# Performance work log

Hardware: AMD Instinct MI355X
Metric: run time of the kernel (lower is better)

The kernel has to match this reference:

```python
import jax, jax.numpy as jnp
import numpy as np

EPS = 1e-6
N_HEADS = 16
N_KV_HEADS = 4
HEAD_DIM = 128
DIM = 2048
SEQ = 2048
BATCH = 2


def _make_freqs_cis(seqlen, head_dim, theta=10000.0):
    inv = 1.0 / (theta ** (jnp.arange(0, head_dim, 2, dtype=jnp.float32) / head_dim))  # [hd/2]
    t = jnp.arange(seqlen, dtype=jnp.float32)
    ang = jnp.outer(t, inv)  # [seq, hd/2]
    return jnp.stack([jnp.cos(ang), jnp.sin(ang)], axis=-1)  # [seq, hd/2, 2]


def setup_inputs() -> dict:
    key = jax.random.key(0)
    k1, k2, k3 = jax.random.split(key, 3)
    std = 0.02
    x = jax.random.normal(k1, (BATCH, SEQ, DIM), dtype=jnp.float32)
    freqs_cis = _make_freqs_cis(SEQ, HEAD_DIM)
    norm_w = jnp.ones((DIM,), dtype=jnp.float32)
    wqkv_w = jax.random.normal(k2, ((N_HEADS + 2 * N_KV_HEADS) * HEAD_DIM, DIM), dtype=jnp.float32) * std
    wo_w = jax.random.normal(k3, (DIM, N_HEADS * HEAD_DIM), dtype=jnp.float32) * std
    return {"x": x, "freqs_cis": freqs_cis, "norm_w": norm_w, "wqkv_w": wqkv_w, "wo_w": wo_w}


def _rope(t, cos, sin):
    # t: [b, s, h, hd] viewed as pairs; cos/sin: [s, hd/2]
    b, s, h, hd = t.shape
    tr = t.reshape(b, s, h, hd // 2, 2)
    xr, xi = tr[..., 0], tr[..., 1]
    c = cos[None, :, None, :]
    sn = sin[None, :, None, :]
    out_r = xr * c - xi * sn
    out_i = xr * sn + xi * c
    return jnp.stack([out_r, out_i], axis=-1).reshape(b, s, h, hd)


def reference(x, freqs_cis, norm_w, wqkv_w, wo_w):
    bs, seqlen, dim = x.shape
    n_rep = N_HEADS // N_KV_HEADS
    # RMSNorm
    xn = x * jax.lax.rsqrt(jnp.mean(x * x, axis=-1, keepdims=True) + EPS) * norm_w
    # fused QKV projection
    qkv = jnp.einsum('bsd,ed->bse', xn, wqkv_w)
    q_sz = N_HEADS * HEAD_DIM
    kv_sz = N_KV_HEADS * HEAD_DIM
    xq = qkv[..., :q_sz].reshape(bs, seqlen, N_HEADS, HEAD_DIM)
    xk = qkv[..., q_sz:q_sz + kv_sz].reshape(bs, seqlen, N_KV_HEADS, HEAD_DIM)
    xv = qkv[..., q_sz + kv_sz:].reshape(bs, seqlen, N_KV_HEADS, HEAD_DIM)
    cos, sin = freqs_cis[..., 0], freqs_cis[..., 1]
    xq = _rope(xq, cos, sin)
    xk = _rope(xk, cos, sin)
    # GQA: group q heads so kv broadcast replaces repeat_kv materialization
    q = xq.transpose(0, 2, 1, 3).reshape(bs, N_KV_HEADS, n_rep, seqlen, HEAD_DIM)
    k = xk.transpose(0, 2, 1, 3)  # [b, g, s, d]
    v = xv.transpose(0, 2, 1, 3)
    scale = 1.0 / jnp.sqrt(jnp.float32(HEAD_DIM))
    scores = jnp.einsum('bgrqd,bgkd->bgrqk', q, k) * scale
    causal = jnp.tril(jnp.ones((seqlen, seqlen), dtype=bool))
    scores = jnp.where(causal, scores, jnp.finfo(scores.dtype).min)
    probs = jax.nn.softmax(scores, axis=-1)
    out = jnp.einsum('bgrqk,bgkd->bgrqd', probs, v)
    out = out.reshape(bs, N_HEADS, seqlen, HEAD_DIM).transpose(0, 2, 1, 3).reshape(bs, seqlen, N_HEADS * HEAD_DIM)
    return jnp.einsum('bse,de->bsd', out, wo_w)
```

## Files before the change

### kernel.cpp

```cpp
#include <hip/hip_runtime.h>
#include <cstdint>
#include <cstddef>

typedef __bf16 bhalf;
typedef __bf16 bhalf8 __attribute__((ext_vector_type(8)));
typedef __bf16 bhalf4 __attribute__((ext_vector_type(4)));
typedef float f32x4 __attribute__((ext_vector_type(4)));
typedef float f32x16 __attribute__((ext_vector_type(16)));

#define RMS_EPS 1e-6f
#define N_HEADS 16
#define N_KV 4
#define HD 128
#define DIM 2048
#define SEQ 2048
#define BATCH 2

static __device__ __forceinline__ f32x4 mfma16(bhalf8 a, bhalf8 b, f32x4 c) {
    return __builtin_amdgcn_mfma_f32_16x16x32_bf16(a, b, c, 0, 0, 0);
}
static __device__ __forceinline__ f32x16 mfma32(bhalf8 a, bhalf8 b, f32x16 c) {
    return __builtin_amdgcn_mfma_f32_32x32x16_bf16(a, b, c, 0, 0, 0);
}

static __device__ __forceinline__ void gload16(const bhalf* g, bhalf* l) {
    __builtin_amdgcn_global_load_lds((const __attribute__((address_space(1))) unsigned int*)g,
                                     (__attribute__((address_space(3))) unsigned int*)l,
                                     16, 0, 0);
}

static __device__ __forceinline__ unsigned cvt_pk_bf16(float a, float b) {
    unsigned r;
    asm volatile("v_cvt_pk_bf16_f32 %0, %1, %2" : "=v"(r) : "v"(a), "v"(b));
    return r;
}
static __device__ __forceinline__ void plane32_swap(unsigned& a, unsigned& b) {
    asm volatile("v_permlane32_swap_b32 %0, %1" : "+v"(a), "+v"(b));
}

__global__ __launch_bounds__(256) void cvt_w(const float* __restrict__ a,
                                             const float* __restrict__ b,
                                             bhalf* __restrict__ dst) {
    size_t i = ((size_t)blockIdx.x * 256 + threadIdx.x) * 4;
    const size_t NQ = (size_t)3072 * 2048;
    float4 v = (i < NQ) ? ((const float4*)a)[i >> 2] : ((const float4*)b)[(i - NQ) >> 2];
    bhalf4 o;
    o[0] = (bhalf)v.x; o[1] = (bhalf)v.y; o[2] = (bhalf)v.z; o[3] = (bhalf)v.w;
    *(bhalf4*)(dst + i) = o;
}

__global__ __launch_bounds__(256) void rmsnorm_k(const float* __restrict__ x,
                                                 const float* __restrict__ w,
                                                 bhalf* __restrict__ xn) {
    const int row = blockIdx.x;
    const int tid = threadIdx.x;
    const float4* xr = (const float4*)(x + (size_t)row * DIM);
    float4 v0 = xr[tid * 2], v1 = xr[tid * 2 + 1];
    float ss = v0.x * v0.x + v0.y * v0.y + v0.z * v0.z + v0.w * v0.w
             + v1.x * v1.x + v1.y * v1.y + v1.z * v1.z + v1.w * v1.w;
    #pragma unroll
    for (int off = 32; off; off >>= 1) ss += __shfl_xor(ss, off, 64);
    __shared__ float red[4];
    if ((tid & 63) == 0) red[tid >> 6] = ss;
    __syncthreads();
    float tot = red[0] + red[1] + red[2] + red[3];
    float scale = rsqrtf(tot * (1.0f / DIM) + RMS_EPS);
    const float4* wr = (const float4*)w;
    float4 w0 = wr[tid * 2], w1 = wr[tid * 2 + 1];
    bhalf8 o;
    o[0] = (bhalf)(v0.x * scale * w0.x); o[1] = (bhalf)(v0.y * scale * w0.y);
    o[2] = (bhalf)(v0.z * scale * w0.z); o[3] = (bhalf)(v0.w * scale * w0.w);
    o[4] = (bhalf)(v1.x * scale * w1.x); o[5] = (bhalf)(v1.y * scale * w1.y);
    o[6] = (bhalf)(v1.z * scale * w1.z); o[7] = (bhalf)(v1.w * scale * w1.w);
    *(bhalf8*)(xn + (size_t)row * DIM + tid * 8) = o;
}

template <typename OutT>
__global__ __launch_bounds__(256) void gemm_abt(const bhalf* __restrict__ A,
                                                const bhalf* __restrict__ B,
                                                OutT* __restrict__ C,
                                                int N, int K) {
    const int tid = threadIdx.x;
    const int wave = tid >> 6, lane = tid & 63;
    const int quad = lane >> 4, r16 = lane & 15;
    const int m0 = blockIdx.y * 128, n0 = blockIdx.x * 128;
    const int wm = (wave >> 1) * 64, wn = (wave & 1) * 64;

    __shared__ __align__(16) bhalf sA[128][32];
    __shared__ __align__(16) bhalf sB[128][32];

    f32x4 acc[4][4];
    #pragma unroll
    for (int i = 0; i < 4; ++i)
        #pragma unroll
        for (int j = 0; j < 4; ++j) acc[i][j] = (f32x4)0.0f;

    const int lrow = lane >> 2;
    const int lcol = (lane & 3) * 8;
    const int arow = 32 * wave + lrow;
    const bhalf* Ap = A + (size_t)(m0 + arow) * K + lcol;
    const bhalf* Bp = B + (size_t)(n0 + arow) * K + lcol;
    const size_t rs16 = (size_t)16 * K;
    bhalf* sAp0 = &sA[32 * wave][0];
    bhalf* sAp1 = &sA[32 * wave + 16][0];
    bhalf* sBp0 = &sB[32 * wave][0];
    bhalf* sBp1 = &sB[32 * wave + 16][0];

    for (int k0 = 0; k0 < K; k0 += 32) {
        __syncthreads();
        gload16(Ap + k0, sAp0);
        gload16(Ap + k0 + rs16, sAp1);
        gload16(Bp + k0, sBp0);
        gload16(Bp + k0 + rs16, sBp1);
        __syncthreads();
        bhalf8 af[4], bfr[4];
        #pragma unroll
        for (int i = 0; i < 4; ++i) af[i]  = *(bhalf8*)&sA[wm + i * 16 + r16][quad * 8];
        #pragma unroll
        for (int j = 0; j < 4; ++j) bfr[j] = *(bhalf8*)&sB[wn + j * 16 + r16][quad * 8];
        #pragma unroll
        for (int i = 0; i < 4; ++i)
            #pragma unroll
            for (int j = 0; j < 4; ++j)
                acc[i][j] = mfma16(af[i], bfr[j], acc[i][j]);
    }

    #pragma unroll
    for (int i = 0; i < 4; ++i) {
        const int rbase = m0 + wm + i * 16 + quad * 4;
        #pragma unroll
        for (int rr = 0; rr < 4; ++rr) {
            OutT* crow = C + (size_t)(rbase + rr) * N + n0 + wn + r16;
            #pragma unroll
            for (int j = 0; j < 4; ++j) crow[j * 16] = (OutT)acc[i][j][rr];
        }
    }
}

__global__ __launch_bounds__(256) void rope_k(const bhalf* __restrict__ qkv,
                                              const float* __restrict__ freqs,
                                              bhalf* __restrict__ qb,
                                              bhalf* __restrict__ kb,
                                              bhalf* __restrict__ vt) {
    const int bs = blockIdx.x;
    const int b = bs >> 11, s = bs & 2047;
    const bhalf* row = qkv + (size_t)bs * 3072;
    const int tid = threadIdx.x;

    {
        const int h = tid >> 4, d20 = (tid & 15) * 4;
        bhalf8 e = *(const bhalf8*)(row + h * HD + d20 * 2);
        const float* fp = freqs + (size_t)s * 128 + d20 * 2;
        float4 f0 = *(const float4*)fp;
        float4 f1 = *(const float4*)(fp + 4);
        bhalf8 o;
        o[0] = (bhalf)((float)e[0] * f0.x - (float)e[1] * f0.y);
        o[1] = (bhalf)((float)e[0] * f0.y + (float)e[1] * f0.x);
        o[2] = (bhalf)((float)e[2] * f0.z - (float)e[3] * f0.w);
        o[3] = (bhalf)((float)e[2] * f0.w + (float)e[3] * f0.z);
        o[4] = (bhalf)((float)e[4] * f1.x - (float)e[5] * f1.y);
        o[5] = (bhalf)((float)e[4] * f1.y + (float)e[5] * f1.x);
        o[6] = (bhalf)((float)e[6] * f1.z - (float)e[7] * f1.w);
        o[7] = (bhalf)((float)e[6] * f1.w + (float)e[7] * f1.z);
        *(bhalf8*)(qb + ((size_t)(b * N_HEADS + h) * SEQ + s) * HD + d20 * 2) = o;
    }
    if (tid < 64) {
        const int kh = tid >> 4, d20 = (tid & 15) * 4;
        bhalf8 e = *(const bhalf8*)(row + 2048 + kh * HD + d20 * 2);
        const float* fp = freqs + (size_t)s * 128 + d20 * 2;
        float4 f0 = *(const float4*)fp;
        float4 f1 = *(const float4*)(fp + 4);
        bhalf8 o;
        o[0] = (bhalf)((float)e[0] * f0.x - (float)e[1] * f0.y);
        o[1] = (bhalf)((float)e[0] * f0.y + (float)e[1] * f0.x);
        o[2] = (bhalf)((float)e[2] * f0.z - (float)e[3] * f0.w);
        o[3] = (bhalf)((float)e[2] * f0.w + (float)e[3] * f0.z);
        o[4] = (bhalf)((float)e[4] * f1.x - (float)e[5] * f1.y);
        o[5] = (bhalf)((float)e[4] * f1.y + (float)e[5] * f1.x);
        o[6] = (bhalf)((float)e[6] * f1.z - (float)e[7] * f1.w);
        o[7] = (bhalf)((float)e[6] * f1.w + (float)e[7] * f1.z);
        *(bhalf8*)(kb + ((size_t)(b * N_KV + kh) * SEQ + s) * HD + d20 * 2) = o;
    }
    for (int e = tid; e < 512; e += 256) {
        const int kh = e >> 7, d = e & 127;
        vt[((size_t)(b * N_KV + kh) * HD + d) * SEQ + s] = row[2560 + e];
    }
}

__global__ __launch_bounds__(256, 2) void attn_k(const bhalf* __restrict__ qb,
                                                 const bhalf* __restrict__ kb,
                                                 const bhalf* __restrict__ vt,
                                                 bhalf* __restrict__ ob) {
    const int tid = threadIdx.x;
    const int wave = tid >> 6, lane = tid & 63;
    const int l31 = lane & 31, h2 = lane >> 5;
    const int qw = wave & 1, kw = wave >> 1;
    const int bid = ((blockIdx.x & 7) << 6) | ((int)blockIdx.x >> 3);
    const int pair = bid & 15;
    const int hh = (bid >> 4) & 15;
    const int b = bid >> 8;
    const int kvh = hh >> 2;

    __shared__ __align__(16) char smem[33792];
    char* const sK = smem;
    char* const sV = smem + 16384;
    float* const mrg = (float*)smem;

    const bhalf* Kbase = kb + (size_t)(b * N_KV + kvh) * SEQ * HD;
    const bhalf* Vbase = vt + (size_t)(b * N_KV + kvh) * HD * SEQ;
    const float SCL2 = 0.08838834764831845f * 1.4426950408889634f;

    const int mbase = (qw * 64 + lane) * 66;
    const int kr = tid >> 4, kce = (tid & 15) * 8;
    const int vr = tid >> 3, vce = (tid & 7) * 8;
    const int kcB = kce * 2, vcB = vce * 2;
    const int Xl = (h2 << 4) ^ ((l31 & 7) << 4);

    for (int phase = 0; phase < 2; ++phase) {
        const int qt = phase ? (31 - pair) : pair;
        const int qrow = qt * 64 + qw * 32 + l31;
        const int qhi = qt * 64 + qw * 32 + 31;

        const bhalf* qbase = qb + (((size_t)(b * N_HEADS + hh) * SEQ) + qrow) * HD;
        bhalf8 qf[8];
        #pragma unroll
        for (int kk = 0; kk < 8; ++kk) {
            bhalf8 q0 = *(const bhalf8*)(qbase + kk * 16 + h2 * 8);
            #pragma unroll
            for (int e = 0; e < 8; ++e) q0[e] = (bhalf)((float)q0[e] * SCL2);
            qf[kk] = q0;
        }

        f32x16 accO[4];
        #pragma unroll
        for (int dt = 0; dt < 4; ++dt) accO[dt] = (f32x16)0.0f;
        float m_i = -1e30f, l_i = 0.0f;

        bhalf8 kreg[4], vreg[4];
        #pragma unroll
        for (int i = 0; i < 4; ++i) {
            kreg[i] = *(const bhalf8*)(Kbase + (size_t)(kr + 16 * i) * HD + kce);
            vreg[i] = *(const bhalf8*)(Vbase + (size_t)(vr + 32 * i) * SEQ + vce);
        }

        for (int kt = 0; kt <= qt; ++kt) {
            __syncthreads();
            #pragma unroll
            for (int i = 0; i < 4; ++i) {
                const int rk = kr + 16 * i;
                *(bhalf8*)(sK + rk * 256 + (kcB ^ ((rk & 7) << 4))) = kreg[i];
                const int rv = vr + 32 * i;
                *(bhalf8*)(sV + rv * 128 + (vcB ^ ((rv & 7) << 4))) = vreg[i];
            }
            __syncthreads();
            if (kt < qt) {
                const int kn = (kt + 1) * 64;
                #pragma unroll
                for (int i = 0; i < 4; ++i) {
                    kreg[i] = *(const bhalf8*)(Kbase + (size_t)(kn + kr + 16 * i) * HD + kce);
                    vreg[i] = *(const bhalf8*)(Vbase + (size_t)(vr + 32 * i) * SEQ + kn + vce);
                }
            }
            if (qhi < kt * 64 + kw * 32) continue;

            f32x16 accS = (f32x16)0.0f;
            const char* kRow = sK + (kw * 32 + l31) * 256;
            #pragma unroll
            for (int kk = 0; kk < 8; ++kk)
                accS = mfma32(*(const bhalf8*)(kRow + ((kk * 32) ^ Xl)), qf[kk], accS);

            if (kt == qt) {
                #pragma unroll
                for (int r = 0; r < 16; ++r) {
                    const int key = kt * 64 + kw * 32 + (r & 3) + 8 * (r >> 2) + 4 * h2;
                    if (key > qrow) accS[r] = -1e30f;
                }
            }

            float mx = -1e30f;
            #pragma unroll
            for (int r = 0; r < 16; ++r) mx = fmaxf(mx, accS[r]);
            mx = fmaxf(mx, __shfl_xor(mx, 32, 64));

            if (!__all(mx <= m_i + 8.0f)) {
                const float mnew = fmaxf(m_i, mx);
                const float alpha = __builtin_amdgcn_exp2f(m_i - mnew);
                m_i = mnew;
                l_i *= alpha;
                #pragma unroll
                for (int dt = 0; dt < 4; ++dt)
                    #pragma unroll
                    for (int r = 0; r < 16; ++r) accO[dt][r] *= alpha;
            }

            float p[16];
            float rs = 0.0f;
            #pragma unroll
            for (int r = 0; r < 16; ++r) {
                p[r] = __builtin_amdgcn_exp2f(accS[r] - m_i);
                rs += p[r];
            }
            rs += __shfl_xor(rs, 32, 64);
            l_i += rs;

            unsigned X0 = cvt_pk_bf16(p[0],  p[1]);
            unsigned X1 = cvt_pk_bf16(p[2],  p[3]);
            unsigned X2 = cvt_pk_bf16(p[4],  p[5]);
            unsigned X3 = cvt_pk_bf16(p[6],  p[7]);
            unsigned X4 = cvt_pk_bf16(p[8],  p[9]);
            unsigned X5 = cvt_pk_bf16(p[10], p[11]);
            unsigned X6 = cvt_pk_bf16(p[12], p[13]);
            unsigned X7 = cvt_pk_bf16(p[14], p[15]);
            plane32_swap(X0, X2);
            plane32_swap(X1, X3);
            plane32_swap(X4, X6);
            plane32_swap(X5, X7);
            union { unsigned u[8]; bhalf8 h[2]; } pk;
            pk.u[0] = X0; pk.u[1] = X1; pk.u[2] = X2; pk.u[3] = X3;
            pk.u[4] = X4; pk.u[5] = X5; pk.u[6] = X6; pk.u[7] = X7;

            #pragma unroll
            for (int kk2 = 0; kk2 < 2; ++kk2) {
                const int cb = (kw << 6) | (kk2 << 5);
                #pragma unroll
                for (int dt = 0; dt < 4; ++dt) {
                    const bhalf8 vfv = *(const bhalf8*)(sV + (dt * 32 + l31) * 128 + (cb ^ Xl));
                    accO[dt] = mfma32(vfv, pk.h[kk2], accO[dt]);
                }
            }
        }

        __syncthreads();
        if (kw == 1) {
            #pragma unroll
            for (int dt = 0; dt < 4; ++dt)
                #pragma unroll
                for (int r = 0; r < 16; ++r) mrg[mbase + dt * 16 + r] = accO[dt][r];
            mrg[mbase + 64] = m_i;
            mrg[mbase + 65] = l_i;
        }
        __syncthreads();
        if (kw == 0) {
            const float m1 = mrg[mbase + 64];
            const float l1 = mrg[mbase + 65];
            const float m = fmaxf(m_i, m1);
            const float b0 = __builtin_amdgcn_exp2f(m_i - m);
            const float b1 = __builtin_amdgcn_exp2f(m1 - m);
            const float inv = 1.0f / (l_i * b0 + l1 * b1);
            bhalf* obase = ob + ((size_t)b * SEQ + qrow) * (size_t)(N_HEADS * HD) + hh * HD;
            #pragma unroll
            for (int dt = 0; dt < 4; ++dt)
                #pragma unroll
                for (int c = 0; c < 4; ++c) {
                    bhalf4 o4;
                    #pragma unroll
                    for (int rr = 0; rr < 4; ++rr) {
                        const float v = accO[dt][c * 4 + rr] * b0 +
                                        mrg[mbase + dt * 16 + c * 4 + rr] * b1;
                        o4[rr] = (bhalf)(v * inv);
                    }
                    *(bhalf4*)(obase + dt * 32 + c * 8 + h2 * 4) = o4;
                }
        }
    }
}

extern "C" void kernel_launch(void* const* d_in, const int* in_sizes, int n_in,
                              void* d_out, int out_size, void* d_ws, size_t ws_size,
                              hipStream_t stream) {
    const float* x      = (const float*)d_in[0];
    const float* freqs  = (const float*)d_in[1];
    const float* norm_w = (const float*)d_in[2];
    const float* wqkv   = (const float*)d_in[3];
    const float* wo     = (const float*)d_in[4];
    float* out = (float*)d_out;

    char* ws = (char*)d_ws;
    bhalf* wqkv_b = (bhalf*)(ws);
    bhalf* wo_b   = (bhalf*)(ws + 12582912);
    bhalf* xn     = (bhalf*)(ws + 20971520);
    bhalf* qkv    = (bhalf*)(ws + 37748736);
    bhalf* qb     = (bhalf*)(ws + 88080384);
    bhalf* kb     = (bhalf*)(ws + 104857600);
    bhalf* vtb    = (bhalf*)(ws + 109051904);
    bhalf* attn   = (bhalf*)(ws + 113246208);

    cvt_w<<<10240, 256, 0, stream>>>(wqkv, wo, wqkv_b);
    rmsnorm_k<<<BATCH * SEQ, 256, 0, stream>>>(x, norm_w, xn);
    gemm_abt<bhalf><<<dim3(24, 32), 256, 0, stream>>>(xn, wqkv_b, qkv, 3072, 2048);
    rope_k<<<BATCH * SEQ, 256, 0, stream>>>(qkv, freqs, qb, kb, vtb);
    attn_k<<<512, 256, 0, stream>>>(qb, kb, vtb, attn);
    gemm_abt<float><<<dim3(16, 32), 256, 0, stream>>>(attn, wo_b, out, 2048, 2048);
}
```

Before: 319.5 us.

## Replace GEMM with 256x256-tile, 512-thread, triple-buffered pipelined kernel

Replaces the 128x128 single-buffered GEMM with a 256x256-tile kernel using 8 waves, a three-stage LDS ring with asynchronous global-to-LDS loads, XOR-swizzled LDS addressing, and block-index remapping for L2 locality. Loads for future k-steps overlap the MFMA work, and s_setprio raises priority during the MFMA bursts. The aim is to raise arithmetic intensity and hide memory latency in the QKV and output projections. Larger tiles mean only 192 and 128 blocks, which may underfill the GPU's compute units, and the kernel needs 96KB of dynamic shared memory.

```diff
diff --git a/kernel.cpp b/kernel.cpp
--- a/kernel.cpp
+++ b/kernel.cpp
@@ -76,61 +76,99 @@
 }
 
 template <typename OutT>
-__global__ __launch_bounds__(256) void gemm_abt(const bhalf* __restrict__ A,
-                                                const bhalf* __restrict__ B,
-                                                OutT* __restrict__ C,
-                                                int N, int K) {
+__global__ __launch_bounds__(512) void gemm256(const bhalf* __restrict__ A,
+                                               const bhalf* __restrict__ B,
+                                               OutT* __restrict__ C,
+                                               int N, int K) {
+    extern __shared__ __align__(16) char smem[];
     const int tid = threadIdx.x;
-    const int wave = tid >> 6, lane = tid & 63;
+    const int wid = tid >> 6, lane = tid & 63;
     const int quad = lane >> 4, r16 = lane & 15;
-    const int m0 = blockIdx.y * 128, n0 = blockIdx.x * 128;
-    const int wm = (wave >> 1) * 64, wn = (wave & 1) * 64;
-
-    __shared__ __align__(16) bhalf sA[128][32];
-    __shared__ __align__(16) bhalf sB[128][32];
-
-    f32x4 acc[4][4];
+    const int wm = wid >> 2, wn = wid & 3;
+
+    const int nx = N >> 8;
+    const int cpx = (int)gridDim.x >> 3;
+    const int bs = (int)blockIdx.x;
+    const int bid = (bs & 7) * cpx + (bs >> 3);
+    const int m0 = (bid / nx) << 8, n0 = (bid % nx) << 8;
+
+    const int srow = wid * 32 + (lane >> 2);
+    const int scol = ((lane & 3) ^ ((lane >> 2) & 3)) << 3;
+    const bhalf* Ast = A + (size_t)(m0 + srow) * K + scol;
+    const bhalf* Bst = B + (size_t)(n0 + srow) * K + scol;
+    const size_t r16K = (size_t)16 * K;
+
+    const int xorr = (r16 & 3) << 4;
+    const int rdA = (wm * 128 + r16) * 64 + ((quad * 16) ^ xorr);
+    const int rdB = (wn * 64 + r16) * 64 + ((quad * 16) ^ xorr);
+
+    char* const sA = smem;
+    char* const sB = smem + 49152;
+
+    f32x4 acc[8][4];
     #pragma unroll
-    for (int i = 0; i < 4; ++i)
+    for (int i = 0; i < 8; ++i)
         #pragma unroll
         for (int j = 0; j < 4; ++j) acc[i][j] = (f32x4)0.0f;
 
-    const int lrow = lane >> 2;
-    const int lcol = (lane & 3) * 8;
-    const int arow = 32 * wave + lrow;
-    const bhalf* Ap = A + (size_t)(m0 + arow) * K + lcol;
-    const bhalf* Bp = B + (size_t)(n0 + arow) * K + lcol;
-    const size_t rs16 = (size_t)16 * K;
-    bhalf* sAp0 = &sA[32 * wave][0];
-    bhalf* sAp1 = &sA[32 * wave + 16][0];
-    bhalf* sBp0 = &sB[32 * wave][0];
-    bhalf* sBp1 = &sB[32 * wave + 16][0];
-
-    for (int k0 = 0; k0 < K; k0 += 32) {
-        __syncthreads();
-        gload16(Ap + k0, sAp0);
-        gload16(Ap + k0 + rs16, sAp1);
-        gload16(Bp + k0, sBp0);
-        gload16(Bp + k0 + rs16, sBp1);
-        __syncthreads();
-        bhalf8 af[4], bfr[4];
-        #pragma unroll
-        for (int i = 0; i < 4; ++i) af[i]  = *(bhalf8*)&sA[wm + i * 16 + r16][quad * 8];
-        #pragma unroll
-        for (int j = 0; j < 4; ++j) bfr[j] = *(bhalf8*)&sB[wn + j * 16 + r16][quad * 8];
+    const int NT = K >> 5;
+
+    #define STAGE256(P, bufbase, t) do {                                          \
+        gload16((P) + (size_t)(t) * 32, (bhalf*)((bufbase) + wid * 2048));        \
+        gload16((P) + (size_t)(t) * 32 + r16K, (bhalf*)((bufbase) + wid * 2048 + 1024)); \
+    } while (0)
+
+    STAGE256(Ast, sA, 0);
+    STAGE256(Bst, sB, 0);
+    STAGE256(Ast, sA + 16384, 1);
+    STAGE256(Bst, sB + 16384, 1);
+    asm volatile("s_waitcnt vmcnt(4)" ::: "memory");
+    __builtin_amdgcn_s_barrier();
+
+    int cur = 0, c2 = 2;
+    for (int t = 0; t < NT; ++t) {
+        char* const bufA = sA + cur * 16384;
+        char* const bufB = sB + cur * 16384;
+        bhalf8 bf[4], afl[4];
+        #pragma unroll
+        for (int j = 0; j < 4; ++j) bf[j] = *(const bhalf8*)(bufB + rdB + j * 1024);
+        #pragma unroll
+        for (int i = 0; i < 4; ++i) afl[i] = *(const bhalf8*)(bufA + rdA + i * 1024);
+        if (t + 2 < NT) STAGE256(Ast, sA + c2 * 16384, t + 2);
+        __builtin_amdgcn_s_barrier();
+        __builtin_amdgcn_s_setprio(1);
         #pragma unroll
         for (int i = 0; i < 4; ++i)
             #pragma unroll
             for (int j = 0; j < 4; ++j)
-                acc[i][j] = mfma16(af[i], bfr[j], acc[i][j]);
-    }
+                acc[i][j] = mfma16(afl[i], bf[j], acc[i][j]);
+        __builtin_amdgcn_s_setprio(0);
+        __builtin_amdgcn_s_barrier();
+        bhalf8 afh[4];
+        #pragma unroll
+        for (int i = 0; i < 4; ++i) afh[i] = *(const bhalf8*)(bufA + rdA + 4096 + i * 1024);
+        if (t + 2 < NT) STAGE256(Bst, sB + c2 * 16384, t + 2);
+        asm volatile("s_waitcnt vmcnt(4)" ::: "memory");
+        __builtin_amdgcn_s_barrier();
+        __builtin_amdgcn_s_setprio(1);
+        #pragma unroll
+        for (int i = 0; i < 4; ++i)
+            #pragma unroll
+            for (int j = 0; j < 4; ++j)
+                acc[i + 4][j] = mfma16(afh[i], bf[j], acc[i + 4][j]);
+        __builtin_amdgcn_s_setprio(0);
+        __builtin_amdgcn_s_barrier();
+        cur = (cur == 2) ? 0 : cur + 1;
+        c2 = (c2 == 2) ? 0 : c2 + 1;
+    }
+    #undef STAGE256
 
     #pragma unroll
-    for (int i = 0; i < 4; ++i) {
-        const int rbase = m0 + wm + i * 16 + quad * 4;
+    for (int i = 0; i < 8; ++i) {
+        const int rbase = m0 + wm * 128 + i * 16 + quad * 4;
         #pragma unroll
         for (int rr = 0; rr < 4; ++rr) {
-            OutT* crow = C + (size_t)(rbase + rr) * N + n0 + wn + r16;
+            OutT* crow = C + (size_t)(rbase + rr) * N + n0 + wn * 64 + r16;
             #pragma unroll
             for (int j = 0; j < 4; ++j) crow[j * 16] = (OutT)acc[i][j][rr];
         }
@@ -385,10 +423,19 @@
     bhalf* vtb    = (bhalf*)(ws + 109051904);
     bhalf* attn   = (bhalf*)(ws + 113246208);
 
+    static bool attr_done = false;
+    if (!attr_done) {
+        hipFuncSetAttribute((const void*)gemm256<bhalf>,
+                            hipFuncAttributeMaxDynamicSharedMemorySize, 98304);
+        hipFuncSetAttribute((const void*)gemm256<float>,
+                            hipFuncAttributeMaxDynamicSharedMemorySize, 98304);
+        attr_done = true;
+    }
+
     cvt_w<<<10240, 256, 0, stream>>>(wqkv, wo, wqkv_b);
     rmsnorm_k<<<BATCH * SEQ, 256, 0, stream>>>(x, norm_w, xn);
-    gemm_abt<bhalf><<<dim3(24, 32), 256, 0, stream>>>(xn, wqkv_b, qkv, 3072, 2048);
+    gemm256<bhalf><<<192, 512, 98304, stream>>>(xn, wqkv_b, qkv, 3072, 2048);
     rope_k<<<BATCH * SEQ, 256, 0, stream>>>(qkv, freqs, qb, kb, vtb);
     attn_k<<<512, 256, 0, stream>>>(qb, kb, vtb, attn);
-    gemm_abt<float><<<dim3(16, 32), 256, 0, stream>>>(attn, wo_b, out, 2048, 2048);
-}
+    gemm256<float><<<128, 512, 98304, stream>>>(attn, wo_b, out, 2048, 2048);
+}
```

Result: no change. 323.6 us (+1.3%).

## Triple-buffer GEMM shared-memory tiles with XOR swizzle and XCD-aware block mapping

Applied to the files above, without the earlier changes.

Rewrites the projection GEMM to use three shared-memory stages, so global loads for tile t+2 are issued while tile t is being computed. It waits with vmcnt instead of a full double barrier, and raises wave priority around the MFMA block. It also adds an XOR swizzle on the shared-memory layout to avoid LDS bank conflicts, and remaps the 1D grid so consecutive tiles land on the same XCD for better L2 reuse. The cost is more LDS per block (48KB), which may lower occupancy, plus reliance on hand-written waitcnt correctness.

```diff
diff --git a/kernel.cpp b/kernel.cpp
--- a/kernel.cpp
+++ b/kernel.cpp
@@ -76,18 +76,34 @@
 }
 
 template <typename OutT>
-__global__ __launch_bounds__(256) void gemm_abt(const bhalf* __restrict__ A,
-                                                const bhalf* __restrict__ B,
-                                                OutT* __restrict__ C,
-                                                int N, int K) {
+__global__ __launch_bounds__(256) void gemm128(const bhalf* __restrict__ A,
+                                               const bhalf* __restrict__ B,
+                                               OutT* __restrict__ C,
+                                               int N, int K) {
     const int tid = threadIdx.x;
-    const int wave = tid >> 6, lane = tid & 63;
+    const int w = tid >> 6, lane = tid & 63;
     const int quad = lane >> 4, r16 = lane & 15;
-    const int m0 = blockIdx.y * 128, n0 = blockIdx.x * 128;
-    const int wm = (wave >> 1) * 64, wn = (wave & 1) * 64;
-
-    __shared__ __align__(16) bhalf sA[128][32];
-    __shared__ __align__(16) bhalf sB[128][32];
+    const int wm = w >> 1, wn = w & 1;
+
+    const int nx = N >> 7;
+    const int cpx = (int)gridDim.x >> 3;
+    const int bs = (int)blockIdx.x;
+    const int bid = (bs & 7) * cpx + (bs >> 3);
+    const int m0 = (bid / nx) << 7, n0 = (bid % nx) << 7;
+
+    __shared__ __align__(16) char smem[49152];
+    char* const sA = smem;
+    char* const sB = smem + 24576;
+
+    const int srow = lane >> 2;
+    const int scol = ((lane & 3) ^ (srow & 3)) << 3;
+    const bhalf* Ast = A + (size_t)(m0 + w * 16 + srow) * K + scol;
+    const bhalf* Bst = B + (size_t)(n0 + w * 16 + srow) * K + scol;
+    const size_t r64K = (size_t)64 * K;
+
+    const int xorr = (r16 & 3) << 4;
+    const int rdA = (wm * 64 + r16) * 64 + ((quad * 16) ^ xorr);
+    const int rdB = (wn * 64 + r16) * 64 + ((quad * 16) ^ xorr);
 
     f32x4 acc[4][4];
     #pragma unroll
@@ -95,42 +111,53 @@
         #pragma unroll
         for (int j = 0; j < 4; ++j) acc[i][j] = (f32x4)0.0f;
 
-    const int lrow = lane >> 2;
-    const int lcol = (lane & 3) * 8;
-    const int arow = 32 * wave + lrow;
-    const bhalf* Ap = A + (size_t)(m0 + arow) * K + lcol;
-    const bhalf* Bp = B + (size_t)(n0 + arow) * K + lcol;
-    const size_t rs16 = (size_t)16 * K;
-    bhalf* sAp0 = &sA[32 * wave][0];
-    bhalf* sAp1 = &sA[32 * wave + 16][0];
-    bhalf* sBp0 = &sB[32 * wave][0];
-    bhalf* sBp1 = &sB[32 * wave + 16][0];
-
-    for (int k0 = 0; k0 < K; k0 += 32) {
-        __syncthreads();
-        gload16(Ap + k0, sAp0);
-        gload16(Ap + k0 + rs16, sAp1);
-        gload16(Bp + k0, sBp0);
-        gload16(Bp + k0 + rs16, sBp1);
-        __syncthreads();
-        bhalf8 af[4], bfr[4];
-        #pragma unroll
-        for (int i = 0; i < 4; ++i) af[i]  = *(bhalf8*)&sA[wm + i * 16 + r16][quad * 8];
-        #pragma unroll
-        for (int j = 0; j < 4; ++j) bfr[j] = *(bhalf8*)&sB[wn + j * 16 + r16][quad * 8];
+    const int NT = K >> 5;
+
+    #define STG128(t, buf) do {                                                        \
+        gload16(Ast + (size_t)(t) * 32,        (bhalf*)(sA + (buf) * 8192 + w * 1024));        \
+        gload16(Ast + (size_t)(t) * 32 + r64K, (bhalf*)(sA + (buf) * 8192 + 4096 + w * 1024)); \
+        gload16(Bst + (size_t)(t) * 32,        (bhalf*)(sB + (buf) * 8192 + w * 1024));        \
+        gload16(Bst + (size_t)(t) * 32 + r64K, (bhalf*)(sB + (buf) * 8192 + 4096 + w * 1024)); \
+    } while (0)
+
+    STG128(0, 0);
+    STG128(1, 1);
+
+    int cur = 0, c2 = 2;
+    for (int t = 0; t < NT; ++t) {
+        if (t + 1 < NT) asm volatile("s_waitcnt vmcnt(4)" ::: "memory");
+        else            asm volatile("s_waitcnt vmcnt(0)" ::: "memory");
+        __builtin_amdgcn_s_barrier();
+
+        char* const bufA = sA + cur * 8192;
+        char* const bufB = sB + cur * 8192;
+        bhalf8 af[4], bf[4];
+        #pragma unroll
+        for (int i = 0; i < 4; ++i) af[i] = *(const bhalf8*)(bufA + rdA + i * 1024);
+        #pragma unroll
+        for (int j = 0; j < 4; ++j) bf[j] = *(const bhalf8*)(bufB + rdB + j * 1024);
+
+        if (t + 2 < NT) STG128(t + 2, c2);
+
+        __builtin_amdgcn_s_setprio(1);
         #pragma unroll
         for (int i = 0; i < 4; ++i)
             #pragma unroll
             for (int j = 0; j < 4; ++j)
-                acc[i][j] = mfma16(af[i], bfr[j], acc[i][j]);
-    }
+                acc[i][j] = mfma16(af[i], bf[j], acc[i][j]);
+        __builtin_amdgcn_s_setprio(0);
+
+        cur = (cur == 2) ? 0 : cur + 1;
+        c2 = (c2 == 2) ? 0 : c2 + 1;
+    }
+    #undef STG128
 
     #pragma unroll
     for (int i = 0; i < 4; ++i) {
-        const int rbase = m0 + wm + i * 16 + quad * 4;
+        const int rbase = m0 + wm * 64 + i * 16 + quad * 4;
         #pragma unroll
         for (int rr = 0; rr < 4; ++rr) {
-            OutT* crow = C + (size_t)(rbase + rr) * N + n0 + wn + r16;
+            OutT* crow = C + (size_t)(rbase + rr) * N + n0 + wn * 64 + r16;
             #pragma unroll
             for (int j = 0; j < 4; ++j) crow[j * 16] = (OutT)acc[i][j][rr];
         }
@@ -387,8 +414,8 @@
 
     cvt_w<<<10240, 256, 0, stream>>>(wqkv, wo, wqkv_b);
     rmsnorm_k<<<BATCH * SEQ, 256, 0, stream>>>(x, norm_w, xn);
-    gemm_abt<bhalf><<<dim3(24, 32), 256, 0, stream>>>(xn, wqkv_b, qkv, 3072, 2048);
+    gemm128<bhalf><<<768, 256, 0, stream>>>(xn, wqkv_b, qkv, 3072, 2048);
     rope_k<<<BATCH * SEQ, 256, 0, stream>>>(qkv, freqs, qb, kb, vtb);
     attn_k<<<512, 256, 0, stream>>>(qb, kb, vtb, attn);
-    gemm_abt<float><<<dim3(16, 32), 256, 0, stream>>>(attn, wo_b, out, 2048, 2048);
-}
+    gemm128<float><<<512, 256, 0, stream>>>(attn, wo_b, out, 2048, 2048);
+}
```

Result: faster. 301.8 us (-5.5%).
